# Kernel tuning notes

Measured on AMD Instinct MI355X. Metric: run time of the kernel, lower is better.

Reference implementation:

```python
import jax, jax.numpy as jnp
import numpy as np

GRID = 16
N = GRID * GRID          # num_nodes = 256
D = 64                   # embed_dim
SPARSITY = 0.8
BATCH = 2048


def setup_inputs() -> dict:
    key = jax.random.key(0)
    ks = jax.random.split(key, 11)
    s1 = 1.0 / np.sqrt(D)          # fan_in of per-node Linears
    s2 = 1.0 / np.sqrt(N * D)      # fan_in of global_pool first Linear
    x = jax.random.normal(ks[0], (BATCH, N * D), dtype=jnp.float32)
    adj_param = jax.random.normal(ks[1], (N, N), dtype=jnp.float32) * 0.1
    W1 = jax.random.uniform(ks[2], (N, D, D), minval=-s1, maxval=s1, dtype=jnp.float32)
    b1 = jax.random.uniform(ks[3], (N, D), minval=-s1, maxval=s1, dtype=jnp.float32)
    W2 = jax.random.uniform(ks[4], (N, D, D), minval=-s1, maxval=s1, dtype=jnp.float32)
    b2 = jax.random.uniform(ks[5], (N, D), minval=-s1, maxval=s1, dtype=jnp.float32)
    gpW1 = jax.random.uniform(ks[6], (N * D, D), minval=-s2, maxval=s2, dtype=jnp.float32)
    gpb1 = jax.random.uniform(ks[7], (D,), minval=-s2, maxval=s2, dtype=jnp.float32)
    gpW2 = jax.random.uniform(ks[8], (D, D // 2), minval=-s1, maxval=s1, dtype=jnp.float32)
    gpb2 = jax.random.uniform(ks[9], (D // 2,), minval=-s1, maxval=s1, dtype=jnp.float32)
    return {"x": x, "adj_param": adj_param, "W1": W1, "b1": b1, "W2": W2, "b2": b2,
            "gpW1": gpW1, "gpb1": gpb1, "gpW2": gpW2, "gpb2": gpb2}


def _adjacency(adj_param):
    adj = jax.nn.sigmoid(adj_param)
    # threshold = sorted(flat adj)[int(sparsity * N*N)], then hard-threshold, then zero diagonal
    thr = jnp.sort(adj.reshape(-1))[int(SPARSITY * N * N)]
    adj = adj * (adj > thr)
    return adj * (1.0 - jnp.eye(N, dtype=adj.dtype))


def reference(x, adj_param, W1, b1, W2, b2, gpW1, gpb1, gpW2, gpb2):
    B = x.shape[0]
    adj = _adjacency(adj_param)
    xn = x.reshape(B, N, D)                                    # [B, N, D]
    # per-node distinct MLP == grouped GEMM with weights [N, D, D]
    h = jax.nn.relu(jnp.einsum('bnd,nde->bne', xn, W1) + b1)   # [B, N, D]
    node = jnp.einsum('bnd,nde->bne', h, W2) + b2              # [B, N, D]
    # adjacency-weighted neighbor sum: mixed[b,i] = sum_j adj[i,j] * node[b,j]
    mixed = jnp.einsum('ij,bjd->bid', adj, node)               # [B, N, D]
    final = 0.5 * mixed + 0.5 * node                           # residual mix
    g = jax.nn.relu(final.reshape(B, N * D) @ gpW1 + gpb1)     # [B, D]
    out = g @ gpW2 + gpb2                                      # [B, D//2]
    return out, adj
```

## Files before the change

kernel.cpp:

```cpp
#include <hip/hip_runtime.h>
#include <math.h>

typedef unsigned int uint;
typedef unsigned short ushort;
typedef short short8 __attribute__((ext_vector_type(8)));
typedef float f32x4 __attribute__((ext_vector_type(4)));

#define B_ 2048
#define N_ 256
#define D_ 64
#define ND_ 16384
#define NN_ 65536
#define KIDX_ 52428u
#define NGROUPS 16

#define WS_W1T    ((size_t)0)
#define WS_W2T    ((size_t)2*1024*1024)
#define WS_EFF    ((size_t)4*1024*1024)
#define WS_GPARTS ((size_t)8*1024*1024)
#define WS_SCAL   ((size_t)16*1024*1024)

__device__ __forceinline__ ushort f2bf(float f) {
    uint u = __float_as_uint(f);
    u += 0x7fffu + ((u >> 16) & 1u);
    return (ushort)(u >> 16);
}
__device__ __forceinline__ float bf2f(ushort u) { return __uint_as_float(((uint)u) << 16); }

__device__ __forceinline__ float sigmoid_exact(float a) {
    float t = (float)exp(-(double)a);
    return 1.0f / (1.0f + t);
}

__device__ __forceinline__ int wfrag_off(int e, int k) {
    return ((((e >> 4) * 2 + (k >> 5)) * 4 + ((k >> 3) & 3)) * 16 + (e & 15)) * 8 + (k & 7);
}

__device__ __forceinline__ int afrag_off(int jl, int i) {
    return (((((jl >> 4) * 8 + (i >> 5)) * 4 + ((i >> 3) & 3)) * 16) + (jl & 15)) * 8 + (i & 7);
}

__global__ __launch_bounds__(1024) void k_cvt_radix(const float* __restrict__ W1,
                                                    const float* __restrict__ W2,
                                                    const float* __restrict__ adj_param,
                                                    ushort* __restrict__ W1f,
                                                    ushort* __restrict__ W2f,
                                                    uint* __restrict__ scal) {
    __shared__ uint SH[16390] __attribute__((aligned(16)));
    int bid = blockIdx.x, tid = threadIdx.x;

    if (bid != 0) {
        int q = tid >> 8, t = tid & 255;
        int m = (bid - 1) * 4 + q;
        ushort* P = (ushort*)SH + q * 4096;
        const float* src = (m < 256) ? W1 + (size_t)m * 4096 : W2 + (size_t)(m - 256) * 4096;
#pragma unroll
        for (int i = 0; i < 16; i++) {
            int idx = i * 256 + t;
            int k = idx >> 6, e = idx & 63;
            P[wfrag_off(e, k)] = f2bf(src[idx]);
        }
        __syncthreads();
        ushort* dst = (m < 256) ? W1f + (size_t)m * 4096 : W2f + (size_t)(m - 256) * 4096;
#pragma unroll
        for (int i = 0; i < 2; i++)
            ((uint4*)dst)[i * 256 + t] = ((const uint4*)P)[i * 256 + t];
        return;
    }

    uint* histL = SH;
    uint* wsum = SH + 16384;
    uint* bc = SH + 16388;
    int lane = tid & 63;
    uint prefix = 0;
    uint rank = KIDX_;
    const uint4* pv = (const uint4*)adj_param;
#pragma unroll 1
    for (int pass = 0; pass < 4; pass++) {
        int shift = 24 - 8 * pass;
        for (int i = tid; i < 256 * 64; i += 1024) histL[i] = 0u;
        __syncthreads();
#pragma unroll 1
        for (int i = 0; i < 16; i++) {
            uint4 b4 = pv[i * 1024 + tid];
#pragma unroll
            for (int c = 0; c < 4; c++) {
                uint bits = (c == 0) ? b4.x : (c == 1) ? b4.y : (c == 2) ? b4.z : b4.w;
                uint key = bits ^ ((bits & 0x80000000u) ? 0xFFFFFFFFu : 0x80000000u);
                bool cand = (pass == 0) || ((key >> (32 - 8 * pass)) == prefix);
                if (cand) atomicAdd(&histL[(((key >> shift) & 0xffu) << 6) + lane], 1u);
            }
        }
        __syncthreads();
        uint s0 = 0, sc = 0;
        if (tid < 256) {
#pragma unroll
            for (int l = 0; l < 64; l++) s0 += histL[(tid << 6) + ((l + tid) & 63)];
            sc = s0;
#pragma unroll
            for (int o = 1; o < 64; o <<= 1) {
                uint t2 = __shfl_up(sc, o, 64);
                if ((tid & 63) >= o) sc += t2;
            }
            if ((tid & 63) == 63) wsum[tid >> 6] = sc;
        }
        __syncthreads();
        if (tid < 256) {
            uint base = 0;
#pragma unroll
            for (int w = 0; w < 4; w++)
                if (w < (tid >> 6)) base += wsum[w];
            uint incl = base + sc;
            uint excl = incl - s0;
            if (excl <= rank && rank < incl) {
                bc[0] = (prefix << 8) | (uint)tid;
                bc[1] = rank - excl;
            }
        }
        __syncthreads();
        prefix = bc[0];
        rank = bc[1];
        __syncthreads();
    }
    if (tid == 0) {
        uint key = prefix;
        uint bits = (key & 0x80000000u) ? (key ^ 0x80000000u) : ~key;
        scal[0] = __float_as_uint(sigmoid_exact(__uint_as_float(bits)));
    }
}

__global__ __launch_bounds__(256) void k_threff(const float* __restrict__ adj_param,
                                                const uint* __restrict__ scal,
                                                const float* __restrict__ gpW1,
                                                float* __restrict__ adj_out,
                                                ushort* __restrict__ effF) {
    __shared__ ushort adjS[16384] __attribute__((aligned(16)));
    __shared__ ushort Bf[16384] __attribute__((aligned(16)));
    int d = blockIdx.x, jt = blockIdx.y, tid = threadIdx.x;
    float thr = __uint_as_float(scal[0]);

    {
        int jl = tid & 63;
        int jglob = jt * 64 + jl;
        int wrow = tid >> 6;
#pragma unroll 1
        for (int i = 0; i < 64; i++) {
            int ir = i * 4 + wrow;
            float s = sigmoid_exact(adj_param[(size_t)ir * 256 + jglob]);
            float v = (s > thr && ir != jglob) ? s : 0.0f;
            adjS[afrag_off(jl, ir)] = f2bf(v);
            if (d == 0) adj_out[(size_t)ir * 256 + jglob] = v;
        }
    }
#pragma unroll
    for (int t = 0; t < 16; t++) {
        int idx = t * 256 + tid;
        int i = idx >> 4;
        int f4 = idx & 15;
        float4 v = *(const float4*)(gpW1 + ((size_t)i * 64 + d) * 64 + f4 * 4);
        int slab = i >> 6, il = i & 63, e0 = f4 * 4;
        Bf[slab * 4096 + wfrag_off(e0 + 0, il)] = f2bf(v.x);
        Bf[slab * 4096 + wfrag_off(e0 + 1, il)] = f2bf(v.y);
        Bf[slab * 4096 + wfrag_off(e0 + 2, il)] = f2bf(v.z);
        Bf[slab * 4096 + wfrag_off(e0 + 3, il)] = f2bf(v.w);
    }
    __syncthreads();
    int wid = tid >> 6, lane = tid & 63, quad = lane >> 4, l16 = lane & 15;
    f32x4 acc[4];
#pragma unroll
    for (int nt = 0; nt < 4; nt++) acc[nt] = (f32x4){0.f, 0.f, 0.f, 0.f};
#pragma unroll
    for (int ks8 = 0; ks8 < 8; ks8++) {
        short8 af = *(const short8*)&adjS[((((wid * 8 + ks8) * 4 + quad) * 16 + l16)) * 8];
        int slab = ks8 >> 1, ks = ks8 & 1;
#pragma unroll
        for (int nt = 0; nt < 4; nt++) {
            short8 bf = *(const short8*)&Bf[slab * 4096 + (((nt * 2 + ks) * 4 + quad) * 16 + l16) * 8];
            acc[nt] = __builtin_amdgcn_mfma_f32_16x16x32_bf16(af, bf, acc[nt], 0, 0, 0);
        }
    }
#pragma unroll
    for (int nt = 0; nt < 4; nt++) {
        int e = nt * 16 + l16;
#pragma unroll
        for (int r = 0; r < 4; r++) {
            int j = jt * 64 + wid * 16 + quad * 4 + r;
            float w = gpW1[((size_t)j * 64 + d) * 64 + e];
            float eff = 0.5f * (acc[nt][r] + w);
            effF[(size_t)j * 4096 + wfrag_off(e, d)] = f2bf(eff);
        }
    }
}

__global__ __launch_bounds__(256, 4) void k_fused(const float* __restrict__ x,
                                                  const ushort* __restrict__ W1f,
                                                  const ushort* __restrict__ W2f,
                                                  const ushort* __restrict__ effF,
                                                  const float* __restrict__ b1,
                                                  const float* __restrict__ b2,
                                                  float* __restrict__ gparts) {
    __shared__ ushort Wf1[4096] __attribute__((aligned(16)));
    __shared__ ushort Wf2[4096] __attribute__((aligned(16)));
    __shared__ ushort Ef[4096] __attribute__((aligned(16)));
    __shared__ ushort St[4][16 * 72];
    int tid = threadIdx.x;
    int g = blockIdx.x, bt = blockIdx.y;
    int wid = tid >> 6, lane = tid & 63, quad = lane >> 4, l16 = lane & 15;
    int rbase = bt * 64 + wid * 16;
    ushort* Sw = &St[wid][0];
    const float* xrow = x + (size_t)(rbase + l16) * ND_ + quad * 8;

    int n0 = g * 16;
    uint4 w1a = ((const uint4*)(W1f + (size_t)n0 * 4096))[tid];
    uint4 w1b = ((const uint4*)(W1f + (size_t)n0 * 4096))[256 + tid];
    uint4 w2a = ((const uint4*)(W2f + (size_t)n0 * 4096))[tid];
    uint4 w2b = ((const uint4*)(W2f + (size_t)n0 * 4096))[256 + tid];
    uint4 ea  = ((const uint4*)(effF + (size_t)n0 * 4096))[tid];
    uint4 eb  = ((const uint4*)(effF + (size_t)n0 * 4096))[256 + tid];
    float4 xr0, xr1, xr2, xr3;
    {
        const float* xp = xrow + (size_t)n0 * 64;
        xr0 = *(const float4*)(xp);
        xr1 = *(const float4*)(xp + 4);
        xr2 = *(const float4*)(xp + 32);
        xr3 = *(const float4*)(xp + 36);
    }
    float b1n[4], b2n[4];
#pragma unroll
    for (int nt = 0; nt < 4; nt++) {
        b1n[nt] = b1[n0 * 64 + nt * 16 + l16];
        b2n[nt] = b2[n0 * 64 + nt * 16 + l16];
    }
    ((uint4*)Wf1)[tid] = w1a;  ((uint4*)Wf1)[256 + tid] = w1b;
    ((uint4*)Wf2)[tid] = w2a;  ((uint4*)Wf2)[256 + tid] = w2b;
    ((uint4*)Ef)[tid]  = ea;   ((uint4*)Ef)[256 + tid]  = eb;

    f32x4 accg[4];
#pragma unroll
    for (int nt = 0; nt < 4; nt++) accg[nt] = (f32x4){0.f, 0.f, 0.f, 0.f};

    __syncthreads();

#pragma unroll 1
    for (int nl = 0; nl < 16; nl++) {
        short8 fa0, fa1;
        {
            short8 a;
            a[0] = (short)f2bf(xr0.x); a[1] = (short)f2bf(xr0.y);
            a[2] = (short)f2bf(xr0.z); a[3] = (short)f2bf(xr0.w);
            a[4] = (short)f2bf(xr1.x); a[5] = (short)f2bf(xr1.y);
            a[6] = (short)f2bf(xr1.z); a[7] = (short)f2bf(xr1.w);
            fa0 = a;
            short8 b;
            b[0] = (short)f2bf(xr2.x); b[1] = (short)f2bf(xr2.y);
            b[2] = (short)f2bf(xr2.z); b[3] = (short)f2bf(xr2.w);
            b[4] = (short)f2bf(xr3.x); b[5] = (short)f2bf(xr3.y);
            b[6] = (short)f2bf(xr3.z); b[7] = (short)f2bf(xr3.w);
            fa1 = b;
        }
        float bias1[4], bias2[4];
#pragma unroll
        for (int nt = 0; nt < 4; nt++) { bias1[nt] = b1n[nt]; bias2[nt] = b2n[nt]; }

        if (nl < 15) {
            int nn = g * 16 + nl + 1;
            w1a = ((const uint4*)(W1f + (size_t)nn * 4096))[tid];
            w1b = ((const uint4*)(W1f + (size_t)nn * 4096))[256 + tid];
            w2a = ((const uint4*)(W2f + (size_t)nn * 4096))[tid];
            w2b = ((const uint4*)(W2f + (size_t)nn * 4096))[256 + tid];
            ea  = ((const uint4*)(effF + (size_t)nn * 4096))[tid];
            eb  = ((const uint4*)(effF + (size_t)nn * 4096))[256 + tid];
            const float* xp = xrow + (size_t)nn * 64;
            xr0 = *(const float4*)(xp);
            xr1 = *(const float4*)(xp + 4);
            xr2 = *(const float4*)(xp + 32);
            xr3 = *(const float4*)(xp + 36);
#pragma unroll
            for (int nt = 0; nt < 4; nt++) {
                b1n[nt] = b1[nn * 64 + nt * 16 + l16];
                b2n[nt] = b2[nn * 64 + nt * 16 + l16];
            }
        }

        f32x4 acc[4];
#pragma unroll
        for (int nt = 0; nt < 4; nt++) acc[nt] = (f32x4){0.f, 0.f, 0.f, 0.f};
#pragma unroll
        for (int nt = 0; nt < 4; nt++) {
            short8 bf = *(const short8*)&Wf1[(((nt * 2 + 0) * 4 + quad) * 16 + l16) * 8];
            acc[nt] = __builtin_amdgcn_mfma_f32_16x16x32_bf16(fa0, bf, acc[nt], 0, 0, 0);
        }
#pragma unroll
        for (int nt = 0; nt < 4; nt++) {
            short8 bf = *(const short8*)&Wf1[(((nt * 2 + 1) * 4 + quad) * 16 + l16) * 8];
            acc[nt] = __builtin_amdgcn_mfma_f32_16x16x32_bf16(fa1, bf, acc[nt], 0, 0, 0);
        }
#pragma unroll
        for (int nt = 0; nt < 4; nt++)
#pragma unroll
            for (int r = 0; r < 4; r++) {
                float h = fmaxf(acc[nt][r] + bias1[nt], 0.0f);
                Sw[(quad * 4 + r) * 72 + nt * 16 + l16] = f2bf(h);
            }
        f32x4 acc2[4];
#pragma unroll
        for (int nt = 0; nt < 4; nt++) acc2[nt] = (f32x4){0.f, 0.f, 0.f, 0.f};
#pragma unroll
        for (int ks = 0; ks < 2; ks++) {
            short8 a2 = *(const short8*)&Sw[l16 * 72 + ks * 32 + quad * 8];
#pragma unroll
            for (int nt = 0; nt < 4; nt++) {
                short8 bf = *(const short8*)&Wf2[(((nt * 2 + ks) * 4 + quad) * 16 + l16) * 8];
                acc2[nt] = __builtin_amdgcn_mfma_f32_16x16x32_bf16(a2, bf, acc2[nt], 0, 0, 0);
            }
        }
#pragma unroll
        for (int nt = 0; nt < 4; nt++)
#pragma unroll
            for (int r = 0; r < 4; r++) {
                float v = acc2[nt][r] + bias2[nt];
                Sw[(quad * 4 + r) * 72 + nt * 16 + l16] = f2bf(v);
            }
#pragma unroll
        for (int ks = 0; ks < 2; ks++) {
            short8 a3 = *(const short8*)&Sw[l16 * 72 + ks * 32 + quad * 8];
#pragma unroll
            for (int nt = 0; nt < 4; nt++) {
                short8 bf = *(const short8*)&Ef[(((nt * 2 + ks) * 4 + quad) * 16 + l16) * 8];
                accg[nt] = __builtin_amdgcn_mfma_f32_16x16x32_bf16(a3, bf, accg[nt], 0, 0, 0);
            }
        }

        if (nl < 15) {
            __syncthreads();
            ((uint4*)Wf1)[tid] = w1a;  ((uint4*)Wf1)[256 + tid] = w1b;
            ((uint4*)Wf2)[tid] = w2a;  ((uint4*)Wf2)[256 + tid] = w2b;
            ((uint4*)Ef)[tid]  = ea;   ((uint4*)Ef)[256 + tid]  = eb;
            __syncthreads();
        }
    }

    float* gp = gparts + ((size_t)g * B_ + bt * 64) * 64;
#pragma unroll
    for (int nt = 0; nt < 4; nt++)
#pragma unroll
        for (int r = 0; r < 4; r++) {
            int b_loc = wid * 16 + quad * 4 + r;
            int e = nt * 16 + l16;
            gp[b_loc * 64 + e] = accg[nt][r];
        }
}

__global__ __launch_bounds__(64) void k_gp2(const float* __restrict__ gparts,
                                            const float* __restrict__ gpb1,
                                            const float* __restrict__ gpW2,
                                            const float* __restrict__ gpb2,
                                            float* __restrict__ out) {
    __shared__ float gs[64];
    int b = blockIdx.x, e = threadIdx.x;
    float s = gpb1[e];
#pragma unroll
    for (int p = 0; p < NGROUPS; p++) s += gparts[((size_t)p * B_ + b) * 64 + e];
    gs[e] = fmaxf(s, 0.0f);
    __syncthreads();
    if (e < 32) {
        float a = gpb2[e];
#pragma unroll 8
        for (int k2 = 0; k2 < 64; k2++) a += gs[k2] * gpW2[k2 * 32 + e];
        out[(size_t)b * 32 + e] = a;
    }
}

extern "C" void kernel_launch(void* const* d_in, const int* in_sizes, int n_in,
                              void* d_out, int out_size, void* d_ws, size_t ws_size,
                              hipStream_t stream) {
    const float* x = (const float*)d_in[0];
    const float* adj_param = (const float*)d_in[1];
    const float* W1 = (const float*)d_in[2];
    const float* b1 = (const float*)d_in[3];
    const float* W2 = (const float*)d_in[4];
    const float* b2 = (const float*)d_in[5];
    const float* gpW1 = (const float*)d_in[6];
    const float* gpb1 = (const float*)d_in[7];
    const float* gpW2 = (const float*)d_in[8];
    const float* gpb2 = (const float*)d_in[9];

    float* out = (float*)d_out;
    float* adj_out = (float*)d_out + NN_;

    char* ws = (char*)d_ws;
    ushort* W1f = (ushort*)(ws + WS_W1T);
    ushort* W2f = (ushort*)(ws + WS_W2T);
    ushort* effF = (ushort*)(ws + WS_EFF);
    float* gparts = (float*)(ws + WS_GPARTS);
    uint* scal = (uint*)(ws + WS_SCAL);

    k_cvt_radix<<<129, 1024, 0, stream>>>(W1, W2, adj_param, W1f, W2f, scal);
    k_threff<<<dim3(64, 4), 256, 0, stream>>>(adj_param, scal, gpW1, adj_out, effF);
    k_fused<<<dim3(NGROUPS, 32), 256, 0, stream>>>(x, W1f, W2f, effF, b1, b2, gparts);
    k_gp2<<<2048, 64, 0, stream>>>(gparts, gpb1, gpW2, gpb2, out);
}
```

Baseline: 287.0 us.

## Split node groups finer, batch adjacency loads, pack four rows per gp2 block

After: 280.4 us. -2.3%, faster.

```diff
diff --git a/kernel.cpp b/kernel.cpp
--- a/kernel.cpp
+++ b/kernel.cpp
@@ -12,13 +12,13 @@
 #define ND_ 16384
 #define NN_ 65536
 #define KIDX_ 52428u
-#define NGROUPS 16
+#define NGROUPS 32
 
 #define WS_W1T    ((size_t)0)
 #define WS_W2T    ((size_t)2*1024*1024)
 #define WS_EFF    ((size_t)4*1024*1024)
 #define WS_GPARTS ((size_t)8*1024*1024)
-#define WS_SCAL   ((size_t)16*1024*1024)
+#define WS_SCAL   ((size_t)24*1024*1024)
 
 __device__ __forceinline__ ushort f2bf(float f) {
     uint u = __float_as_uint(f);
@@ -144,12 +144,19 @@
         int jglob = jt * 64 + jl;
         int wrow = tid >> 6;
 #pragma unroll 1
-        for (int i = 0; i < 64; i++) {
-            int ir = i * 4 + wrow;
-            float s = sigmoid_exact(adj_param[(size_t)ir * 256 + jglob]);
-            float v = (s > thr && ir != jglob) ? s : 0.0f;
-            adjS[afrag_off(jl, ir)] = f2bf(v);
-            if (d == 0) adj_out[(size_t)ir * 256 + jglob] = v;
+        for (int i = 0; i < 16; i++) {
+            float p[4];
+#pragma unroll
+            for (int u = 0; u < 4; u++)
+                p[u] = adj_param[(size_t)((i * 4 + u) * 4 + wrow) * 256 + jglob];
+#pragma unroll
+            for (int u = 0; u < 4; u++) {
+                int ir = (i * 4 + u) * 4 + wrow;
+                float s = sigmoid_exact(p[u]);
+                float v = (s > thr && ir != jglob) ? s : 0.0f;
+                adjS[afrag_off(jl, ir)] = f2bf(v);
+                if (d == 0) adj_out[(size_t)ir * 256 + jglob] = v;
+            }
         }
     }
 #pragma unroll
@@ -210,7 +217,7 @@
     ushort* Sw = &St[wid][0];
     const float* xrow = x + (size_t)(rbase + l16) * ND_ + quad * 8;
 
-    int n0 = g * 16;
+    int n0 = g * 8;
     uint4 w1a = ((const uint4*)(W1f + (size_t)n0 * 4096))[tid];
     uint4 w1b = ((const uint4*)(W1f + (size_t)n0 * 4096))[256 + tid];
     uint4 w2a = ((const uint4*)(W2f + (size_t)n0 * 4096))[tid];
@@ -242,7 +249,7 @@
     __syncthreads();
 
 #pragma unroll 1
-    for (int nl = 0; nl < 16; nl++) {
+    for (int nl = 0; nl < 8; nl++) {
         short8 fa0, fa1;
         {
             short8 a;
@@ -262,8 +269,8 @@
 #pragma unroll
         for (int nt = 0; nt < 4; nt++) { bias1[nt] = b1n[nt]; bias2[nt] = b2n[nt]; }
 
-        if (nl < 15) {
-            int nn = g * 16 + nl + 1;
+        if (nl < 7) {
+            int nn = g * 8 + nl + 1;
             w1a = ((const uint4*)(W1f + (size_t)nn * 4096))[tid];
             w1b = ((const uint4*)(W1f + (size_t)nn * 4096))[256 + tid];
             w2a = ((const uint4*)(W2f + (size_t)nn * 4096))[tid];
@@ -331,7 +338,7 @@
             }
         }
 
-        if (nl < 15) {
+        if (nl < 7) {
             __syncthreads();
             ((uint4*)Wf1)[tid] = w1a;  ((uint4*)Wf1)[256 + tid] = w1b;
             ((uint4*)Wf2)[tid] = w2a;  ((uint4*)Wf2)[256 + tid] = w2b;
@@ -351,23 +358,26 @@
         }
 }
 
-__global__ __launch_bounds__(64) void k_gp2(const float* __restrict__ gparts,
-                                            const float* __restrict__ gpb1,
-                                            const float* __restrict__ gpW2,
-                                            const float* __restrict__ gpb2,
-                                            float* __restrict__ out) {
-    __shared__ float gs[64];
-    int b = blockIdx.x, e = threadIdx.x;
+__global__ __launch_bounds__(256) void k_gp2(const float* __restrict__ gparts,
+                                             const float* __restrict__ gpb1,
+                                             const float* __restrict__ gpW2,
+                                             const float* __restrict__ gpb2,
+                                             float* __restrict__ out) {
+    __shared__ float gs[4][64];
+    int b0 = blockIdx.x * 4, tid = threadIdx.x;
+    int r = tid >> 6, e = tid & 63;
     float s = gpb1[e];
 #pragma unroll
-    for (int p = 0; p < NGROUPS; p++) s += gparts[((size_t)p * B_ + b) * 64 + e];
-    gs[e] = fmaxf(s, 0.0f);
+    for (int p = 0; p < NGROUPS; p++)
+        s += gparts[((size_t)p * B_ + b0 + r) * 64 + e];
+    gs[r][e] = fmaxf(s, 0.0f);
     __syncthreads();
-    if (e < 32) {
-        float a = gpb2[e];
+    if (tid < 128) {
+        int rr = tid >> 5, o = tid & 31;
+        float a = gpb2[o];
 #pragma unroll 8
-        for (int k2 = 0; k2 < 64; k2++) a += gs[k2] * gpW2[k2 * 32 + e];
-        out[(size_t)b * 32 + e] = a;
+        for (int k2 = 0; k2 < 64; k2++) a += gs[rr][k2] * gpW2[k2 * 32 + o];
+        out[(size_t)(b0 + rr) * 32 + o] = a;
     }
 }
 
@@ -398,5 +408,5 @@
     k_cvt_radix<<<129, 1024, 0, stream>>>(W1, W2, adj_param, W1f, W2f, scal);
     k_threff<<<dim3(64, 4), 256, 0, stream>>>(adj_param, scal, gpW1, adj_out, effF);
     k_fused<<<dim3(NGROUPS, 32), 256, 0, stream>>>(x, W1f, W2f, effF, b1, b2, gparts);
-    k_gp2<<<2048, 64, 0, stream>>>(gparts, gpb1, gpW2, gpb2, out);
-}
+    k_gp2<<<512, 256, 0, stream>>>(gparts, gpb1, gpW2, gpb2, out);
+}
```
